# Kernel optimization log

Hardware: AMD Instinct MI355X
Metric: run time of the kernel (lower is better)

## Reference

```python
import jax, jax.numpy as jnp
import numpy as np

DK = 8.0          # sqrt(in_dim) with in_dim = 64
BN_SCALE = 1.0 / np.float32(np.sqrt(1.0 + 1e-5))  # eval-mode BatchNorm3d at init (mean=0, var=1, gamma=1, beta=0)


def conv3d(x, w, b):
    # x: [B,Cin,D1,D2,D3], w: [Cout,Cin,3,3,3], stride 1, padding 1 == SAME
    y = jax.lax.conv_general_dilated(
        x, w, window_strides=(1, 1, 1), padding='SAME',
        dimension_numbers=('NCDHW', 'OIDHW', 'NCDHW'))
    return y + b[None, :, None, None, None]


def axial(qm, km, vm):
    # qm/km/vm: [B,C,S,L,M]; attention over L with keys along M-contraction.
    # scores[b,c,s,i,j] = sum_m (q/dk)[...,i,m] * k[...,j,m]  -> [B,C,S,L,L]
    s = jnp.einsum('bcsim,bcsjm->bcsij', qm / DK, km)
    # torch nn.Softmax(dim=1) applied to [N,L,L] normalizes over the FIRST L axis (i)
    a = jax.nn.softmax(s, axis=-2)
    return jnp.einsum('bcsij,bcsjm->bcsim', a, vm)


def setup_inputs() -> dict:
    key = jax.random.key(0)
    ks = jax.random.split(key, 5)
    B, C, H, W, D = 2, 64, 64, 64, 64
    x = jax.random.normal(ks[0], (B, C, H, W, D), jnp.float32)
    Wq = jax.random.normal(ks[1], (C, C, 3, 3, 3), jnp.float32) * 0.02
    Wk = jax.random.normal(ks[2], (C, C, 3, 3, 3), jnp.float32) * 0.02
    Wv = jax.random.normal(ks[3], (C, C, 3, 3, 3), jnp.float32) * 0.02
    Wc = jax.random.normal(ks[4], (C, 3 * C, 3, 3, 3), jnp.float32) * 0.02
    z = jnp.zeros((C,), jnp.float32)
    return {"x": x, "Wq": Wq, "bq": z, "Wk": Wk, "bk": z,
            "Wv": Wv, "bv": z, "Wc": Wc, "bc": z}


def reference(x, Wq, bq, Wk, bk, Wv, bv, Wc, bc):
    # projections (dropout is inactive at inference)
    q = conv3d(x, Wq, bq)
    k = conv3d(x, Wk, bk)
    v = conv3d(x, Wv, bv)
    P = jnp.transpose

    # ---- loop over D slices: attend over H (and over W in the transposed pass) ----
    pa = (0, 1, 4, 2, 3)        # [B,C,D,H,W]
    ava = axial(P(q, pa), P(k, pa), P(v, pa))          # [B,C,D,H,W]
    ava = P(ava, (0, 1, 3, 4, 2))                       # -> [B,C,H,W,D]
    pb = (0, 1, 4, 3, 2)        # [B,C,D,W,H]
    ava1 = axial(P(q, pb), P(k, pb), P(v, pb))          # [B,C,D,W,H]
    ava1 = P(ava1, (0, 1, 4, 3, 2))                     # -> [B,C,H,W,D]
    AVa = (ava + ava1) * 0.5

    # ---- loop over W slices: attend over H (and over D) ----
    pc = (0, 1, 3, 2, 4)        # [B,C,W,H,D]
    avb = axial(P(q, pc), P(k, pc), P(v, pc))           # [B,C,W,H,D]
    avb = P(avb, (0, 1, 3, 2, 4))                       # -> [B,C,H,W,D]
    pd = (0, 1, 3, 4, 2)        # [B,C,W,D,H]
    avb1 = axial(P(q, pd), P(k, pd), P(v, pd))          # [B,C,W,D,H]
    avb1 = P(avb1, (0, 1, 4, 2, 3))                     # -> [B,C,H,W,D]
    AVb = (avb + avb1) * 0.5

    # ---- loop over H slices: attend over W (and over D) ----
    avc = axial(q, k, v)                                 # [B,C,H,W,D]
    pe = (0, 1, 2, 4, 3)        # [B,C,H,D,W]
    avc1 = axial(P(q, pe), P(k, pe), P(v, pe))          # [B,C,H,D,W]
    avc1 = P(avc1, (0, 1, 2, 4, 3))                     # -> [B,C,H,W,D]
    AVc = (avc + avc1) * 0.5

    cat = jnp.concatenate([AVa, AVb, AVc], axis=1)      # [B,3C,H,W,D]
    y = jax.nn.relu(conv3d(cat, Wc, bc) * BN_SCALE)     # Conv_3x3x3: conv + BN(eval) + ReLU
    y = y * BN_SCALE                                    # outer BatchNorm3d (eval)
    return y + q
```

## Files before the change

kernel.cpp:

```cpp
#include <hip/hip_runtime.h>

typedef unsigned short u16;
typedef unsigned int u32;
typedef __attribute__((ext_vector_type(8))) __bf16 bf16x8;
typedef __attribute__((ext_vector_type(4))) float f32x4;
typedef __attribute__((ext_vector_type(4))) u16 u16x4;

#define VOL 262144

__device__ __forceinline__ u16 f2bf(float f) {
  u32 u = __builtin_bit_cast(u32, f);
  u32 r = u + 0x7FFFu + ((u >> 16) & 1u);
  return (u16)(r >> 16);
}
__device__ __forceinline__ float bf2f(u16 h) {
  return __builtin_bit_cast(float, ((u32)h) << 16);
}
__device__ __forceinline__ bf16x8 ldsfrag(const u16* p) { return *(const bf16x8*)p; }

__device__ __forceinline__ void gload16(const u16* g, u16* l) {
  __builtin_amdgcn_global_load_lds(
      (const __attribute__((address_space(1))) u32*)g,
      (__attribute__((address_space(3))) u32*)l, 16, 0, 0);
}

__device__ __forceinline__ int swA(int row, int col) {
  return row * 64 + (col ^ (((row ^ (row >> 3)) & 7) << 3));
}

__global__ __launch_bounds__(256) void swz_qkv(const float* __restrict__ Wq,
    const float* __restrict__ Wk, const float* __restrict__ Wv, u16* __restrict__ out) {
  int idx = blockIdx.x * 256 + threadIdx.x;
  if (idx >= 54 * 12 * 64 * 8) return;
  int jj = idx & 7;
  int lane = (idx >> 3) & 63;
  int t = idx >> 9;
  int nf = t % 12, s = t / 12;
  int dh = s / 18, sub = s % 18;
  int dw = sub / 6, dd = (sub >> 1) % 3, c32 = sub & 1;
  int coutg = nf * 16 + (lane & 15);
  int cin = c32 * 32 + (lane >> 4) * 8 + jj;
  const float* W = (coutg < 64) ? Wq : ((coutg < 128) ? Wk : Wv);
  int c = coutg & 63;
  out[idx] = f2bf(W[(c * 64 + cin) * 27 + dh * 9 + dw * 3 + dd]);
}

__global__ __launch_bounds__(256) void swz_c(const float* __restrict__ Wc, u16* __restrict__ out) {
  int idx = blockIdx.x * 256 + threadIdx.x;
  if (idx >= 162 * 4 * 64 * 8) return;
  int jj = idx & 7;
  int lane = (idx >> 3) & 63;
  int nf = (idx >> 9) & 3;
  int s = idx >> 11;
  int dh = s / 54, rem = s % 54;
  int t = rem / 18, sub = rem % 18;
  int dw = sub / 6, dd = (sub >> 1) % 3, c32 = sub & 1;
  int cout = nf * 16 + (lane & 15);
  int cin = t * 64 + c32 * 32 + (lane >> 4) * 8 + jj;
  out[idx] = f2bf(Wc[(cout * 192 + cin) * 27 + dh * 9 + dw * 3 + dd]);
}

__global__ __launch_bounds__(256, 4) void xcvt(const float* __restrict__ x, u16* __restrict__ xcl) {
  __shared__ __align__(16) u16 tile[4096];
  int id = blockIdx.x;
  int b = id >> 12;
  int t = threadIdx.x;
  int c0 = (t & 31) * 2, d0 = (t >> 5) * 8;
  const float* p0 = x + (size_t)(b * 64 + c0) * VOL + (size_t)(id & 4095) * 64 + d0;
  float4 r00 = *(const float4*)p0;
  float4 r01 = *(const float4*)(p0 + 4);
  float4 r10 = *(const float4*)(p0 + VOL);
  float4 r11 = *(const float4*)(p0 + VOL + 4);
  float a0[8] = {r00.x, r00.y, r00.z, r00.w, r01.x, r01.y, r01.z, r01.w};
  float a1[8] = {r10.x, r10.y, r10.z, r10.w, r11.x, r11.y, r11.z, r11.w};
#pragma unroll
  for (int i = 0; i < 8; ++i) {
    int d = d0 + i;
    *(u32*)&tile[d * 64 + (c0 ^ ((d & 7) << 3))] =
        (u32)f2bf(a0[i]) | ((u32)f2bf(a1[i]) << 16);
  }
  __syncthreads();
  u16* dst = xcl + ((size_t)id << 12);
  *(uint4*)&dst[t * 16] = *(const uint4*)&tile[t * 16];
  *(uint4*)&dst[t * 16 + 8] = *(const uint4*)&tile[t * 16 + 8];
}

__global__ __launch_bounds__(512, 2) void conv_qkv(const u16* __restrict__ xcl,
    const u16* __restrict__ BQ, const float* __restrict__ bq, const float* __restrict__ bk,
    const float* __restrict__ bv, u16* __restrict__ qb, u16* __restrict__ kb,
    u16* __restrict__ vb) {
  __shared__ __align__(16) u16 xT[2 * 16896];
  int tid = threadIdx.x;
  int id = blockIdx.x;
  int lin = (id & 7) * 512 + (id >> 3);
  int b = lin >> 11, h = (lin >> 5) & 63, w0 = (lin & 31) * 2;
  int wave = tid >> 6, lane = tid & 63, r = lane & 15, g = lane >> 4;
  int mhalf = wave >> 2, nq = wave & 3;
  {
    int tl = tid >> 7, rs = (tid >> 6) & 1, ci = tid & 63;
    int off = tl * 4224 + rs * 65 * 64 + ci;
    xT[off] = 0;
    xT[16896 + off] = 0;
  }
  if (w0 == 0) {
    *(uint4*)&xT[64 + tid * 8] = uint4{0, 0, 0, 0};
    *(uint4*)&xT[16896 + 64 + tid * 8] = uint4{0, 0, 0, 0};
  }
  if (w0 == 62) {
    *(uint4*)&xT[3 * 4224 + 64 + tid * 8] = uint4{0, 0, 0, 0};
    *(uint4*)&xT[16896 + 3 * 4224 + 64 + tid * 8] = uint4{0, 0, 0, 0};
  }
  int tw = wave >> 1, half = wave & 1;
  int wws = w0 + tw - 1;
  bool doload = (unsigned)wws < 64u;

  f32x4 acc[4][3];
#pragma unroll
  for (int i = 0; i < 4; ++i)
#pragma unroll
    for (int j = 0; j < 3; ++j)
#pragma unroll
      for (int e = 0; e < 4; ++e) acc[i][j][e] = 0.0f;

  int dhlo = (h == 0) ? 1 : 0, dhhi = (h == 63) ? 1 : 2;
  if (doload) {
    int hh = h + dhlo - 1;
    const u16* gp = xcl + (((size_t)(b * 64 + hh) * 64 + wws) << 12) + (half << 11) + (lane << 3);
    u16* lp = &xT[tw * 4224 + 64 + half * 2048];
#pragma unroll
    for (int j = 0; j < 4; ++j) gload16(gp + j * 512, lp + j * 512);
  }
  int cur = 0;
  for (int dh = dhlo; dh <= dhhi; ++dh) {
    __syncthreads();
    if (dh < dhhi && doload) {
      int hh = h + dh;
      const u16* gp =
          xcl + (((size_t)(b * 64 + hh) * 64 + wws) << 12) + (half << 11) + (lane << 3);
      u16* lp = &xT[(cur ^ 1) * 16896 + tw * 4224 + 64 + half * 2048];
#pragma unroll
      for (int j = 0; j < 4; ++j) gload16(gp + j * 512, lp + j * 512);
    }
    const u16* Bbase = BQ + ((size_t)(dh * 18) * 12 + nq * 3) * 512 + (size_t)lane * 8;
    int bufE = cur * 16896;
    for (int sub = 0; sub < 18; ++sub) {
      int dw = sub / 6, dd = (sub >> 1) % 3, c32 = sub & 1;
      int colb = c32 * 32 + g * 8;
      int wwi = mhalf + dw;
      bf16x8 A[4];
#pragma unroll
      for (int l = 0; l < 4; ++l) {
        int dpos = l * 16 + r + dd;
        A[l] = ldsfrag(&xT[bufE + wwi * 4224 + dpos * 64 + (colb ^ (((dpos - 1) & 7) << 3))]);
      }
      const u16* Bp = Bbase + (size_t)sub * 12 * 512;
#pragma unroll
      for (int nf = 0; nf < 3; ++nf) {
        bf16x8 Bf = *(const bf16x8*)(Bp + nf * 512);
#pragma unroll
        for (int l = 0; l < 4; ++l)
          acc[l][nf] = __builtin_amdgcn_mfma_f32_16x16x32_bf16(A[l], Bf, acc[l][nf], 0, 0, 0);
      }
    }
    cur ^= 1;
  }
#pragma unroll
  for (int nf = 0; nf < 3; ++nf) {
    int coutg = (nq * 3 + nf) * 16 + r;
    int ten = coutg >> 6, c = coutg & 63;
    u16* dst = (ten == 0) ? qb : ((ten == 1) ? kb : vb);
    const float* bias = (ten == 0) ? bq : ((ten == 1) ? bk : bv);
    float bsv = bias[c];
#pragma unroll
    for (int l = 0; l < 4; ++l) {
      int d0 = l * 16 + g * 4;
      int idx = (b * 64 + c) * VOL + h * 4096 + (w0 + mhalf) * 64 + d0;
      u16x4 o;
#pragma unroll
      for (int jj = 0; jj < 4; ++jj) o[jj] = f2bf(acc[l][nf][jj] + bsv);
      *(u16x4*)(dst + idx) = o;
    }
  }
}

__global__ __launch_bounds__(256, 6) void ktranspose(const u16* __restrict__ src,
    u16* __restrict__ dst, int P, int Q) {
  __shared__ __align__(16) u16 tile[64 * 72];
  int tid = threadIdx.x;
  int id = blockIdx.x;
  int bc = id >> 6, t = id & 63;
  int qt = Q >> 6;
  int p0 = (t / qt) * 64, q0 = (t % qt) * 64;
  const u16* s = src + (size_t)bc * VOL;
  u16* d = dst + (size_t)bc * VOL;
#pragma unroll
  for (int it = 0; it < 2; ++it) {
    int c = tid + 256 * it;
    int i2 = c >> 3, sg = c & 7;
    *(uint4*)&tile[i2 * 72 + ((sg * 8) ^ (((i2 >> 3) & 7) << 3))] =
        *(const uint4*)&s[(size_t)(p0 + i2) * Q + q0 + sg * 8];
  }
  __syncthreads();
  int j = tid >> 2, ms = tid & 3;
  u16 vals[16];
#pragma unroll
  for (int ii = 0; ii < 16; ++ii) {
    int row = ms * 16 + ii;
    vals[ii] = tile[row * 72 + (j ^ (((row >> 3) & 7) << 3))];
  }
  uint4 o0, o1;
  o0.x = (u32)vals[0] | ((u32)vals[1] << 16);
  o0.y = (u32)vals[2] | ((u32)vals[3] << 16);
  o0.z = (u32)vals[4] | ((u32)vals[5] << 16);
  o0.w = (u32)vals[6] | ((u32)vals[7] << 16);
  o1.x = (u32)vals[8] | ((u32)vals[9] << 16);
  o1.y = (u32)vals[10] | ((u32)vals[11] << 16);
  o1.z = (u32)vals[12] | ((u32)vals[13] << 16);
  o1.w = (u32)vals[14] | ((u32)vals[15] << 16);
  size_t drow = (size_t)(q0 + j) * P + p0 + ms * 16;
  *(uint4*)&d[drow] = o0;
  *(uint4*)&d[drow + 8] = o1;
}

__global__ __launch_bounds__(256, 2) void attn_pair(const u16* __restrict__ q,
    const u16* __restrict__ k, const u16* __restrict__ v, u16* __restrict__ dst,
    int uStride, int sMul) {
  __shared__ __align__(16) u16 sm[6 * 4096];
  u16* LQ = sm;             u16* LK = sm + 4096;      u16* LV = sm + 2 * 4096;
  u16* LQT = sm + 3 * 4096; u16* LKT = sm + 4 * 4096; u16* LVT = sm + 5 * 4096;
  u16* A1 = LK;
  u16* A2 = LKT;
  int tid = threadIdx.x;
  int id = blockIdx.x;
  int bc = id >> 6, sidx = id & 63;
  size_t base = (size_t)bc * VOL + (size_t)sidx * sMul;
  int wave = tid >> 6, lane = tid & 63, r = lane & 15, g = lane >> 4;
  int pairid = tid >> 3, seg = tid & 7;
  int u0 = pairid * 2;
  const u16* srcs[3] = {q, k, v};
  u16* Ln_[3] = {LQ, LK, LV};
  u16* Lt_[3] = {LQT, LKT, LVT};
#pragma unroll
  for (int t3 = 0; t3 < 3; ++t3) {
    const u16* p = srcs[t3] + base + (size_t)u0 * uStride + seg * 8;
    uint4 ra = *(const uint4*)p;
    uint4 rb = *(const uint4*)(p + uStride);
    *(uint4*)&Ln_[t3][swA(u0, seg * 8)] = ra;
    *(uint4*)&Ln_[t3][swA(u0 + 1, seg * 8)] = rb;
    union { uint4 vv; u16 ss[8]; } Ua, Ub;
    Ua.vv = ra; Ub.vv = rb;
#pragma unroll
    for (int vi = 0; vi < 8; ++vi) {
      int vvx = seg * 8 + vi;
      *(u32*)&Lt_[t3][swA(vvx, u0)] = (u32)Ua.ss[vi] | ((u32)Ub.ss[vi] << 16);
    }
  }
  __syncthreads();
  int row0 = wave * 16;
  f32x4 s1[4], s2[4];
#pragma unroll
  for (int nf = 0; nf < 4; ++nf)
#pragma unroll
    for (int e = 0; e < 4; ++e) { s1[nf][e] = 0.f; s2[nf][e] = 0.f; }
#pragma unroll
  for (int ks = 0; ks < 2; ++ks) {
    int cb = ks * 32 + g * 8;
    bf16x8 aK = ldsfrag(&LK[swA(row0 + r, cb)]);
    bf16x8 aKT = ldsfrag(&LKT[swA(row0 + r, cb)]);
#pragma unroll
    for (int nf = 0; nf < 4; ++nf) {
      bf16x8 bQ = ldsfrag(&LQ[swA(nf * 16 + r, cb)]);
      bf16x8 bQT = ldsfrag(&LQT[swA(nf * 16 + r, cb)]);
      s1[nf] = __builtin_amdgcn_mfma_f32_16x16x32_bf16(aK, bQ, s1[nf], 0, 0, 0);
      s2[nf] = __builtin_amdgcn_mfma_f32_16x16x32_bf16(aKT, bQT, s2[nf], 0, 0, 0);
    }
  }
  __syncthreads();
#pragma unroll
  for (int m2 = 0; m2 < 2; ++m2) {
    f32x4* ss = m2 ? s2 : s1;
    u16* Adst = m2 ? A2 : A1;
#pragma unroll
    for (int jj = 0; jj < 4; ++jj) {
      float mx = fmaxf(fmaxf(ss[0][jj], ss[1][jj]), fmaxf(ss[2][jj], ss[3][jj]));
      mx = fmaxf(mx, __shfl_xor(mx, 1, 64));
      mx = fmaxf(mx, __shfl_xor(mx, 2, 64));
      mx = fmaxf(mx, __shfl_xor(mx, 4, 64));
      mx = fmaxf(mx, __shfl_xor(mx, 8, 64));
      float p0 = __expf((ss[0][jj] - mx) * 0.125f);
      float p1 = __expf((ss[1][jj] - mx) * 0.125f);
      float p2 = __expf((ss[2][jj] - mx) * 0.125f);
      float p3 = __expf((ss[3][jj] - mx) * 0.125f);
      float sum = p0 + p1 + p2 + p3;
      sum += __shfl_xor(sum, 1, 64);
      sum += __shfl_xor(sum, 2, 64);
      sum += __shfl_xor(sum, 4, 64);
      sum += __shfl_xor(sum, 8, 64);
      float inv = 1.0f / sum;
      ss[0][jj] = p0 * inv; ss[1][jj] = p1 * inv; ss[2][jj] = p2 * inv; ss[3][jj] = p3 * inv;
    }
    int j0 = row0 + g * 4;
#pragma unroll
    for (int nf = 0; nf < 4; ++nf) {
      int i = nf * 16 + r;
      int a0 = swA(i, j0);
      *(u32*)&Adst[a0]     = (u32)f2bf(ss[nf][0]) | ((u32)f2bf(ss[nf][1]) << 16);
      *(u32*)&Adst[a0 + 2] = (u32)f2bf(ss[nf][2]) | ((u32)f2bf(ss[nf][3]) << 16);
    }
  }
  __syncthreads();
  f32x4 o[4];
#pragma unroll
  for (int nf = 0; nf < 4; ++nf)
#pragma unroll
    for (int e = 0; e < 4; ++e) o[nf][e] = 0.f;
#pragma unroll
  for (int ks = 0; ks < 2; ++ks) {
    int cb = ks * 32 + g * 8;
    bf16x8 aA = ldsfrag(&A1[swA(row0 + r, cb)]);
    bf16x8 aV = ldsfrag(&LV[swA(row0 + r, cb)]);
#pragma unroll
    for (int nf = 0; nf < 4; ++nf) {
      bf16x8 bVT = ldsfrag(&LVT[swA(nf * 16 + r, cb)]);
      bf16x8 bA2 = ldsfrag(&A2[swA(nf * 16 + r, cb)]);
      o[nf] = __builtin_amdgcn_mfma_f32_16x16x32_bf16(aA, bVT, o[nf], 0, 0, 0);
      o[nf] = __builtin_amdgcn_mfma_f32_16x16x32_bf16(aV, bA2, o[nf], 0, 0, 0);
    }
  }
#pragma unroll
  for (int nf = 0; nf < 4; ++nf) {
    int vv = nf * 16 + r;
#pragma unroll
    for (int jj = 0; jj < 4; ++jj) {
      int u = row0 + g * 4 + jj;
      dst[base + (size_t)u * uStride + vv] = f2bf(o[nf][jj] * 0.5f);
    }
  }
}

__global__ __launch_bounds__(512, 2) void conv_final(const u16* __restrict__ AVa,
    const u16* __restrict__ AVb, const u16* __restrict__ AVc, const u16* __restrict__ BCw,
    const float* __restrict__ bcb, const u16* __restrict__ qb, float* __restrict__ out) {
  __shared__ __align__(16) u16 xT[6 * 66 * 72];
  int tid = threadIdx.x;
  int id = blockIdx.x;
  int lin = (id & 7) * 256 + (id >> 3);
  int b = lin >> 10, h = (lin >> 4) & 63, w0 = (lin & 15) * 4;
  int wave = tid >> 6, lane = tid & 63, r = lane & 15, g = lane >> 4;
  int mw = wave >> 1, nw = wave & 1;
  int pairid = tid >> 3, seg = tid & 7;
  if (tid < 384) {
    int wwi = tid >> 6, ci = tid & 63;
    xT[(wwi * 66 + 0) * 72 + ci] = 0;
    xT[(wwi * 66 + 65) * 72 + ci] = 0;
  }
  f32x4 acc[4][2];
#pragma unroll
  for (int i = 0; i < 4; ++i)
#pragma unroll
    for (int j = 0; j < 2; ++j)
#pragma unroll
      for (int e = 0; e < 4; ++e) acc[i][j][e] = 0.f;

  for (int dh = 0; dh < 3; ++dh) {
    int hh = h + dh - 1;
    if ((unsigned)hh >= 64u) continue;
    for (int t = 0; t < 3; ++t) {
      const u16* sp = (t == 0) ? AVa : ((t == 1) ? AVb : AVc);
      __syncthreads();
#pragma unroll
      for (int pi = 0; pi < 3; ++pi) {
        int pair = pairid + 64 * pi;
        int wwi = pair >> 5, cin0 = (pair & 31) * 2;
        int ww = w0 + wwi - 1;
        uint4 ra{}, rb{};
        if ((unsigned)ww < 64u) {
          const u16* p = sp + (size_t)(b * 64 + cin0) * VOL + hh * 4096 + ww * 64 + seg * 8;
          ra = *(const uint4*)p;
          rb = *(const uint4*)(p + VOL);
        }
        union { uint4 vv; u16 ss[8]; } Ua, Ub;
        Ua.vv = ra; Ub.vv = rb;
        int rowb = wwi * 66;
#pragma unroll
        for (int di = 0; di < 8; ++di) {
          int dpos = seg * 8 + di + 1;
          *(u32*)&xT[(rowb + dpos) * 72 + (cin0 ^ (((dpos >> 3) & 7) << 3))] =
              (u32)Ua.ss[di] | ((u32)Ub.ss[di] << 16);
        }
      }
      __syncthreads();
      for (int sub = 0; sub < 18; ++sub) {
        int dw = sub / 6, dd = (sub >> 1) % 3, c32 = sub & 1;
        int colb = c32 * 32 + g * 8;
        int wwi = mw + dw;
        bf16x8 A[4];
#pragma unroll
        for (int dq = 0; dq < 4; ++dq) {
          int dpos = dq * 16 + r + dd;
          A[dq] = ldsfrag(&xT[(wwi * 66 + dpos) * 72 + (colb ^ (((dpos >> 3) & 7) << 3))]);
        }
        const u16* Bp = BCw + ((size_t)(((dh * 3 + t) * 18 + sub) * 4 + nw * 2) * 64 + lane) * 8;
#pragma unroll
        for (int nf = 0; nf < 2; ++nf) {
          bf16x8 Bf = *(const bf16x8*)(Bp + nf * 512);
#pragma unroll
          for (int dq = 0; dq < 4; ++dq)
            acc[dq][nf] = __builtin_amdgcn_mfma_f32_16x16x32_bf16(A[dq], Bf, acc[dq][nf], 0, 0, 0);
        }
      }
    }
  }
  const float S = 0.9999950000374997f;
#pragma unroll
  for (int nf = 0; nf < 2; ++nf) {
    int cout = (nw * 2 + nf) * 16 + r;
    float bsv = bcb[cout];
#pragma unroll
    for (int dq = 0; dq < 4; ++dq) {
      int d0 = dq * 16 + g * 4;
      int idx = (b * 64 + cout) * VOL + h * 4096 + (w0 + mw) * 64 + d0;
      u16x4 qv = *(const u16x4*)(qb + idx);
      float4 ov;
      float t0 = (acc[dq][nf][0] + bsv) * S; t0 = t0 > 0.f ? t0 : 0.f; ov.x = t0 * S + bf2f(qv[0]);
      float t1 = (acc[dq][nf][1] + bsv) * S; t1 = t1 > 0.f ? t1 : 0.f; ov.y = t1 * S + bf2f(qv[1]);
      float t2 = (acc[dq][nf][2] + bsv) * S; t2 = t2 > 0.f ? t2 : 0.f; ov.z = t2 * S + bf2f(qv[2]);
      float t3 = (acc[dq][nf][3] + bsv) * S; t3 = t3 > 0.f ? t3 : 0.f; ov.w = t3 * S + bf2f(qv[3]);
      *(float4*)(out + idx) = ov;
    }
  }
}

extern "C" void kernel_launch(void* const* d_in, const int* in_sizes, int n_in,
                              void* d_out, int out_size, void* d_ws, size_t ws_size,
                              hipStream_t stream) {
  const float* x  = (const float*)d_in[0];
  const float* Wq = (const float*)d_in[1];
  const float* bq = (const float*)d_in[2];
  const float* Wk = (const float*)d_in[3];
  const float* bk = (const float*)d_in[4];
  const float* Wv = (const float*)d_in[5];
  const float* bv = (const float*)d_in[6];
  const float* Wc = (const float*)d_in[7];
  const float* bc = (const float*)d_in[8];
  float* out = (float*)d_out;
  u16* ws = (u16*)d_ws;
  const size_t T = (size_t)33554432;
  u16* qb = ws;
  u16* kb = ws + T;
  u16* vb = ws + 2 * T;
  u16* qT = ws + 3 * T;
  u16* kT = ws + 4 * T;
  u16* vT = ws + 5 * T;
  u16* xcl = ws + 6 * T;
  u16* avaT = ws + 6 * T;
  u16* BQ = ws + 7 * T;
  u16* BC = BQ + 331776;
  u16* AVa = qT;
  u16* AVb = kT;
  u16* AVc = vT;

  swz_qkv<<<1296, 256, 0, stream>>>(Wq, Wk, Wv, BQ);
  swz_c<<<1296, 256, 0, stream>>>(Wc, BC);
  xcvt<<<8192, 256, 0, stream>>>(x, xcl);
  conv_qkv<<<4096, 512, 0, stream>>>(xcl, BQ, bq, bk, bv, qb, kb, vb);
  ktranspose<<<8192, 256, 0, stream>>>(qb, qT, 4096, 64);
  ktranspose<<<8192, 256, 0, stream>>>(kb, kT, 4096, 64);
  ktranspose<<<8192, 256, 0, stream>>>(vb, vT, 4096, 64);
  attn_pair<<<8192, 256, 0, stream>>>(qT, kT, vT, avaT, 64, 4096);
  ktranspose<<<8192, 256, 0, stream>>>(avaT, AVa, 64, 4096);
  attn_pair<<<8192, 256, 0, stream>>>(qb, kb, vb, AVb, 4096, 64);
  attn_pair<<<8192, 256, 0, stream>>>(qb, kb, vb, AVc, 64, 4096);
  conv_final<<<2048, 512, 0, stream>>>(AVa, AVb, AVc, BC, bc, qb, out);
}
```

Before: 1.005 ms.

## Repack attention outputs channels-last so conv_final loads tiles via direct global-to-LDS

Adds two repack kernels that turn each attention output into a channels-last [B,H,W,D,C] bf16 layout, replacing the old transpose for AVa and adding one for AVb and AVc. conv_final now fills its LDS input tile with global_load_lds 16-byte copies using a new swizzle, instead of gathering strided per-channel loads and scattering 32-bit words into LDS. This is meant to cut the uncoalesced load and LDS scatter cost in the final convolution, in exchange for two extra full-volume repack passes over memory.

```diff
diff --git a/kernel.cpp b/kernel.cpp
--- a/kernel.cpp
+++ b/kernel.cpp
@@ -7,6 +7,7 @@
 typedef __attribute__((ext_vector_type(4))) u16 u16x4;
 
 #define VOL 262144
+#define TSZ ((size_t)33554432)
 
 __device__ __forceinline__ u16 f2bf(float f) {
   u32 u = __builtin_bit_cast(u32, f);
@@ -83,6 +84,66 @@
   u16* dst = xcl + ((size_t)id << 12);
   *(uint4*)&dst[t * 16] = *(const uint4*)&tile[t * 16];
   *(uint4*)&dst[t * 16 + 8] = *(const uint4*)&tile[t * 16 + 8];
+}
+
+__global__ __launch_bounds__(256, 4) void repackA(const u16* __restrict__ src, u16* __restrict__ dst) {
+  __shared__ __align__(16) u16 T[64 * 4 * 72];
+  int j = blockIdx.x;
+  int b = j >> 10, h = (j >> 4) & 63, d0 = (j & 15) * 4;
+  int tid = threadIdx.x;
+  int kk = d0 & 4;
+#pragma unroll
+  for (int k = 0; k < 8; ++k) {
+    int chunk = tid + 256 * k;
+    int row = chunk >> 3, woct = chunk & 7;
+    int c = row >> 2, dd = row & 3;
+    uint4 v = *(const uint4*)&src[(size_t)(b * 64 + c) * VOL + (size_t)(d0 + dd) * 4096 +
+                                  h * 64 + woct * 8];
+    union { uint4 u; u16 s[8]; } U; U.u = v;
+    int d7 = kk + dd;
+#pragma unroll
+    for (int wi = 0; wi < 8; ++wi) {
+      T[(woct * 8 + wi) * 288 + dd * 72 + (c ^ ((d7 ^ wi) << 3))] = U.s[wi];
+    }
+  }
+  __syncthreads();
+#pragma unroll
+  for (int k = 0; k < 8; ++k) {
+    int cn = tid + 256 * k;
+    int w = cn >> 5, rem = cn & 31;
+    int dd = rem >> 3, j8 = rem & 7;
+    uint4 v = *(const uint4*)&T[w * 288 + dd * 72 + ((j8 ^ (w & 7)) << 3)];
+    *(uint4*)&dst[(size_t)((b * 64 + h) * 64 + w) * 4096 + (d0 + dd) * 64 + j8 * 8] = v;
+  }
+}
+
+__global__ __launch_bounds__(256, 4) void repackB(const u16* __restrict__ src, u16* __restrict__ dst) {
+  __shared__ __align__(16) u16 T[4 * 64 * 72];
+  int j = blockIdx.x;
+  int b = j >> 10, h = (j >> 4) & 63, w0 = (j & 15) * 4;
+  int tid = threadIdx.x;
+#pragma unroll
+  for (int k = 0; k < 8; ++k) {
+    int chunk = tid + 256 * k;
+    int row = chunk >> 3, doct = chunk & 7;
+    int c = row >> 2, wi2 = row & 3;
+    uint4 v = *(const uint4*)&src[(size_t)(b * 64 + c) * VOL + h * 4096 + (w0 + wi2) * 64 +
+                                  doct * 8];
+    union { uint4 u; u16 s[8]; } U; U.u = v;
+#pragma unroll
+    for (int di = 0; di < 8; ++di) {
+      T[wi2 * 4608 + (doct * 8 + di) * 72 + (c ^ ((di ^ wi2) << 3))] = U.s[di];
+    }
+  }
+  __syncthreads();
+#pragma unroll
+  for (int k = 0; k < 8; ++k) {
+    int cn = tid + 256 * k;
+    int wi2 = cn >> 9, rem = cn & 511;
+    int d = rem >> 3, j8 = rem & 7;
+    uint4 v = *(const uint4*)&T[wi2 * 4608 + d * 72 + ((j8 ^ wi2) << 3)];
+    *(uint4*)&dst[(size_t)((b * 64 + h) * 64 + w0 + wi2) * 4096 + d * 64 + j8 * 8] = v;
+  }
 }
 
 __global__ __launch_bounds__(512, 2) void conv_qkv(const u16* __restrict__ xcl,
@@ -338,22 +399,29 @@
   }
 }
 
-__global__ __launch_bounds__(512, 2) void conv_final(const u16* __restrict__ AVa,
-    const u16* __restrict__ AVb, const u16* __restrict__ AVc, const u16* __restrict__ BCw,
-    const float* __restrict__ bcb, const u16* __restrict__ qb, float* __restrict__ out) {
-  __shared__ __align__(16) u16 xT[6 * 66 * 72];
+__global__ __launch_bounds__(512, 2) void conv_final(const u16* __restrict__ avcl,
+    const u16* __restrict__ BCw, const float* __restrict__ bcb,
+    const u16* __restrict__ qb, float* __restrict__ out) {
+  __shared__ __align__(16) u16 xT[6 * 4224];
   int tid = threadIdx.x;
   int id = blockIdx.x;
   int lin = (id & 7) * 256 + (id >> 3);
   int b = lin >> 10, h = (lin >> 4) & 63, w0 = (lin & 15) * 4;
   int wave = tid >> 6, lane = tid & 63, r = lane & 15, g = lane >> 4;
   int mw = wave >> 1, nw = wave & 1;
-  int pairid = tid >> 3, seg = tid & 7;
-  if (tid < 384) {
-    int wwi = tid >> 6, ci = tid & 63;
-    xT[(wwi * 66 + 0) * 72 + ci] = 0;
-    xT[(wwi * 66 + 65) * 72 + ci] = 0;
-  }
+  for (int z = tid; z < 768; z += 512) {
+    int tl = z >> 7, rs = (z >> 6) & 1, ci = z & 63;
+    xT[tl * 4224 + rs * 65 * 64 + ci] = 0;
+  }
+  if (w0 == 0) *(uint4*)&xT[64 + tid * 8] = uint4{0, 0, 0, 0};
+  if (w0 == 60) *(uint4*)&xT[5 * 4224 + 64 + tid * 8] = uint4{0, 0, 0, 0};
+
+  int tw1 = wave >> 1, hf1 = wave & 1;
+  int tw2 = 4 + (wave >> 1), hf2 = wave & 1;
+  int ww1 = w0 + tw1 - 1, ww2 = w0 + tw2 - 1;
+  bool dl1 = (unsigned)ww1 < 64u;
+  bool dl2 = (wave < 4) && ((unsigned)ww2 < 64u);
+
   f32x4 acc[4][2];
 #pragma unroll
   for (int i = 0; i < 4; ++i)
@@ -366,30 +434,22 @@
     int hh = h + dh - 1;
     if ((unsigned)hh >= 64u) continue;
     for (int t = 0; t < 3; ++t) {
-      const u16* sp = (t == 0) ? AVa : ((t == 1) ? AVb : AVc);
       __syncthreads();
-#pragma unroll
-      for (int pi = 0; pi < 3; ++pi) {
-        int pair = pairid + 64 * pi;
-        int wwi = pair >> 5, cin0 = (pair & 31) * 2;
-        int ww = w0 + wwi - 1;
-        uint4 ra{}, rb{};
-        if ((unsigned)ww < 64u) {
-          const u16* p = sp + (size_t)(b * 64 + cin0) * VOL + hh * 4096 + ww * 64 + seg * 8;
-          ra = *(const uint4*)p;
-          rb = *(const uint4*)(p + VOL);
-        }
-        union { uint4 vv; u16 ss[8]; } Ua, Ub;
-        Ua.vv = ra; Ub.vv = rb;
-        int rowb = wwi * 66;
-#pragma unroll
-        for (int di = 0; di < 8; ++di) {
-          int dpos = seg * 8 + di + 1;
-          *(u32*)&xT[(rowb + dpos) * 72 + (cin0 ^ (((dpos >> 3) & 7) << 3))] =
-              (u32)Ua.ss[di] | ((u32)Ub.ss[di] << 16);
-        }
+      const u16* tbase = avcl + (size_t)t * TSZ;
+      if (dl1) {
+        const u16* gp = tbase + (((size_t)(b * 64 + hh) * 64 + ww1) << 12) + (hf1 << 11) + (lane << 3);
+        u16* lp = &xT[tw1 * 4224 + 64 + hf1 * 2048];
+#pragma unroll
+        for (int j = 0; j < 4; ++j) gload16(gp + j * 512, lp + j * 512);
+      }
+      if (dl2) {
+        const u16* gp = tbase + (((size_t)(b * 64 + hh) * 64 + ww2) << 12) + (hf2 << 11) + (lane << 3);
+        u16* lp = &xT[tw2 * 4224 + 64 + hf2 * 2048];
+#pragma unroll
+        for (int j = 0; j < 4; ++j) gload16(gp + j * 512, lp + j * 512);
       }
       __syncthreads();
+      const u16* Bbase = BCw + ((size_t)((dh * 3 + t) * 18) * 4 + nw * 2) * 512 + (size_t)lane * 8;
       for (int sub = 0; sub < 18; ++sub) {
         int dw = sub / 6, dd = (sub >> 1) % 3, c32 = sub & 1;
         int colb = c32 * 32 + g * 8;
@@ -398,9 +458,9 @@
 #pragma unroll
         for (int dq = 0; dq < 4; ++dq) {
           int dpos = dq * 16 + r + dd;
-          A[dq] = ldsfrag(&xT[(wwi * 66 + dpos) * 72 + (colb ^ (((dpos >> 3) & 7) << 3))]);
+          A[dq] = ldsfrag(&xT[wwi * 4224 + dpos * 64 + (colb ^ (((dpos - 1) & 7) << 3))]);
         }
-        const u16* Bp = BCw + ((size_t)(((dh * 3 + t) * 18 + sub) * 4 + nw * 2) * 64 + lane) * 8;
+        const u16* Bp = Bbase + (size_t)sub * 4 * 512;
 #pragma unroll
         for (int nf = 0; nf < 2; ++nf) {
           bf16x8 Bf = *(const bf16x8*)(Bp + nf * 512);
@@ -445,31 +505,29 @@
   const float* bc = (const float*)d_in[8];
   float* out = (float*)d_out;
   u16* ws = (u16*)d_ws;
-  const size_t T = (size_t)33554432;
   u16* qb = ws;
-  u16* kb = ws + T;
-  u16* vb = ws + 2 * T;
-  u16* qT = ws + 3 * T;
-  u16* kT = ws + 4 * T;
-  u16* vT = ws + 5 * T;
-  u16* xcl = ws + 6 * T;
-  u16* avaT = ws + 6 * T;
-  u16* BQ = ws + 7 * T;
+  u16* kb = ws + TSZ;
+  u16* vb = ws + 2 * TSZ;
+  u16* qT = ws + 3 * TSZ;
+  u16* kT = ws + 4 * TSZ;
+  u16* vT = ws + 5 * TSZ;
+  u16* X  = ws + 6 * TSZ;
+  u16* BQ = ws + 7 * TSZ;
   u16* BC = BQ + 331776;
-  u16* AVa = qT;
-  u16* AVb = kT;
-  u16* AVc = vT;
+  u16* avcl = qT;
 
   swz_qkv<<<1296, 256, 0, stream>>>(Wq, Wk, Wv, BQ);
   swz_c<<<1296, 256, 0, stream>>>(Wc, BC);
-  xcvt<<<8192, 256, 0, stream>>>(x, xcl);
-  conv_qkv<<<4096, 512, 0, stream>>>(xcl, BQ, bq, bk, bv, qb, kb, vb);
+  xcvt<<<8192, 256, 0, stream>>>(x, X);
+  conv_qkv<<<4096, 512, 0, stream>>>(X, BQ, bq, bk, bv, qb, kb, vb);
   ktranspose<<<8192, 256, 0, stream>>>(qb, qT, 4096, 64);
   ktranspose<<<8192, 256, 0, stream>>>(kb, kT, 4096, 64);
   ktranspose<<<8192, 256, 0, stream>>>(vb, vT, 4096, 64);
-  attn_pair<<<8192, 256, 0, stream>>>(qT, kT, vT, avaT, 64, 4096);
-  ktranspose<<<8192, 256, 0, stream>>>(avaT, AVa, 64, 4096);
-  attn_pair<<<8192, 256, 0, stream>>>(qb, kb, vb, AVb, 4096, 64);
-  attn_pair<<<8192, 256, 0, stream>>>(qb, kb, vb, AVc, 64, 4096);
-  conv_final<<<2048, 512, 0, stream>>>(AVa, AVb, AVc, BC, bc, qb, out);
-}
+  attn_pair<<<8192, 256, 0, stream>>>(qT, kT, vT, X, 64, 4096);
+  repackA<<<2048, 256, 0, stream>>>(X, avcl);
+  attn_pair<<<8192, 256, 0, stream>>>(qb, kb, vb, X, 4096, 64);
+  repackB<<<2048, 256, 0, stream>>>(X, avcl + TSZ);
+  attn_pair<<<8192, 256, 0, stream>>>(qb, kb, vb, X, 64, 4096);
+  repackB<<<2048, 256, 0, stream>>>(X, avcl + 2 * TSZ);
+  conv_final<<<2048, 512, 0, stream>>>(avcl, BC, bc, qb, out);
+}
```

After: 1.060 ms. 1.05x slower.
